# Performance work log

Measured on AMD Instinct MI355X. Metric: run time of the kernel, lower is better.

## Reference

```python
import jax, jax.numpy as jnp
import numpy as np

N_NODES = 100000
N_EDGES = 3200000
D_IN = 128


def setup_inputs() -> dict:
    key = jax.random.key(0)
    k1, k2, k3, k4 = jax.random.split(key, 4)
    x = jax.random.normal(k1, (N_NODES, D_IN), dtype=jnp.float32)
    edge_index = jax.random.randint(k2, (2, N_EDGES), 0, N_NODES, dtype=jnp.int64)
    W1 = jax.random.normal(k3, (D_IN, 16), dtype=jnp.float32) * (1.0 / np.sqrt(D_IN))
    b1 = jnp.zeros((16,), dtype=jnp.float32)
    W2 = jax.random.normal(k4, (16, 2), dtype=jnp.float32) * (1.0 / np.sqrt(16))
    b2 = jnp.zeros((2,), dtype=jnp.float32)
    return {"x": x, "edge_index": edge_index, "W1": W1, "b1": b1, "W2": W2, "b2": b2}


def _gcn_norm(edge_index, n_nodes):
    # Add self-loops, then symmetric degree normalization (PyG gcn_norm).
    loops = jnp.arange(n_nodes, dtype=edge_index.dtype)
    row = jnp.concatenate([edge_index[0], loops])  # source
    col = jnp.concatenate([edge_index[1], loops])  # target
    ones = jnp.ones(row.shape[0], dtype=jnp.float32)
    deg = jax.ops.segment_sum(ones, col, num_segments=n_nodes)
    dis = jnp.where(deg > 0, jax.lax.rsqrt(deg), 0.0)  # deg^{-1/2}
    norm = dis[row] * dis[col]  # [E+N]
    return row, col, norm


def _gcn_conv(x, row, col, norm, W, b, n_nodes):
    h = x @ W  # transform first (PyG order): [N, out]
    msgs = h[row] * norm[:, None]  # gather from source, scale
    agg = jax.ops.segment_sum(msgs, col, num_segments=n_nodes)  # scatter-add to target
    return agg + b


def reference(x, edge_index, W1, b1, W2, b2):
    n = x.shape[0]
    row, col, norm = _gcn_norm(edge_index, n)
    h = _gcn_conv(x, row, col, norm, W1, b1, n)
    h = jax.nn.relu(h)
    h = _gcn_conv(h, row, col, norm, W2, b2, n)
    return jax.nn.log_softmax(h, axis=1)
```

## Files before the change

kernel.cpp:

```cpp
#include <hip/hip_runtime.h>
#include <hip/hip_fp16.h>

#define DIN 128
#define BSH 7
#define BSIZE 128
#define NBMAX 800
#define CAP 4480
#define CHUNK 6656
#define EPT 13
#define PB 512
#define PZ 0xAAAAAAAAu

struct PlaceSmem {
    int pk[CHUNK];
    unsigned short bkid[CHUNK];
    int lcnt[NBMAX], lstart[NBMAX], gofs[NBMAX], lcur[NBMAX];
    int sst[16];
};
struct HSmem {
    float xs[64 * 132];
    float wt[16 * 132];
};
union MegaSmem {
    PlaceSmem p;
    HSmem h;
};

__global__ __launch_bounds__(PB, 6) void mega_kernel(const int* __restrict__ row,
                                                     const int* __restrict__ col,
                                                     const float* __restrict__ x,
                                                     const float* __restrict__ W1,
                                                     unsigned* __restrict__ cur,
                                                     int* __restrict__ sp,
                                                     __half* __restrict__ hp,
                                                     int E, int N, int NB, int PBLKS) {
    __shared__ MegaSmem sm;
    int t = threadIdx.x;
    int bid = blockIdx.x;

    if (bid < PBLKS) {
        int e0 = bid * CHUNK;
        int cnt = min(CHUNK, E - e0);
        bool full = (cnt == CHUNK);
        for (int i = t; i < NBMAX; i += PB) { sm.p.lcnt[i] = 0; sm.p.lcur[i] = 0; }
        __syncthreads();
        int cv[EPT], rv[EPT];
        if (full) {
            #pragma unroll
            for (int k = 0; k < EPT; k++) cv[k] = col[e0 + t + k * PB];
            #pragma unroll
            for (int k = 0; k < EPT; k++) rv[k] = row[e0 + t + k * PB];
            #pragma unroll
            for (int k = 0; k < EPT; k++) atomicAdd(&sm.p.lcnt[cv[k] >> BSH], 1);
        } else {
            for (int i = t; i < cnt; i += PB)
                atomicAdd(&sm.p.lcnt[col[e0 + i] >> BSH], 1);
        }
        __syncthreads();
        int b2i = t * 2;
        int v0 = (b2i + 0 < NBMAX) ? sm.p.lcnt[b2i + 0] : 0;
        int v1 = (b2i + 1 < NBMAX) ? sm.p.lcnt[b2i + 1] : 0;
        unsigned g0 = 0, g1 = 0;
        if (b2i + 0 < NB && v0) g0 = atomicAdd(&cur[b2i + 0], (unsigned)v0) - PZ;
        if (b2i + 1 < NB && v1) g1 = atomicAdd(&cur[b2i + 1], (unsigned)v1) - PZ;
        int tot = v0 + v1;
        int lane = t & 63, w = t >> 6;
        int sc = tot;
        #pragma unroll
        for (int d = 1; d < 64; d <<= 1) {
            int up = __shfl_up(sc, d);
            if (lane >= d) sc += up;
        }
        if (lane == 63) sm.p.sst[w] = sc;
        __syncthreads();
        if (t < 64) {
            int v = (lane < 8) ? sm.p.sst[lane] : 0;
            #pragma unroll
            for (int d = 1; d < 8; d <<= 1) {
                int up = __shfl_up(v, d);
                if (lane >= d) v += up;
            }
            if (lane < 8) sm.p.sst[8 + lane] = v;
        }
        __syncthreads();
        int wpre = (w > 0) ? sm.p.sst[8 + w - 1] : 0;
        int ex = sc + wpre - tot;
        if (b2i + 0 < NBMAX) sm.p.lstart[b2i + 0] = ex;
        if (b2i + 1 < NBMAX) sm.p.lstart[b2i + 1] = ex + v0;
        if (b2i + 0 < NB) sm.p.gofs[b2i + 0] = (b2i + 0) * CAP + (int)g0 - ex;
        if (b2i + 1 < NB) sm.p.gofs[b2i + 1] = (b2i + 1) * CAP + (int)g1 - (ex + v0);
        __syncthreads();
        if (full) {
            #pragma unroll
            for (int k = 0; k < EPT; k++) {
                int cc = cv[k];
                int b  = cc >> BSH;
                int rk = atomicAdd(&sm.p.lcur[b], 1);
                int pos = sm.p.lstart[b] + rk;
                sm.p.pk[pos]   = ((cc & (BSIZE - 1)) << 17) | rv[k];
                sm.p.bkid[pos] = (unsigned short)b;
            }
            __syncthreads();
            #pragma unroll
            for (int k = 0; k < EPT; k++) {
                int i = t + k * PB;
                sp[sm.p.gofs[sm.p.bkid[i]] + i] = sm.p.pk[i];
            }
        } else {
            for (int i = t; i < cnt; i += PB) {
                int r  = row[e0 + i];
                int cc = col[e0 + i];
                int b  = cc >> BSH;
                int rk = atomicAdd(&sm.p.lcur[b], 1);
                int pos = sm.p.lstart[b] + rk;
                sm.p.pk[pos]   = ((cc & (BSIZE - 1)) << 17) | r;
                sm.p.bkid[pos] = (unsigned short)b;
            }
            __syncthreads();
            for (int i = t; i < cnt; i += PB)
                sp[sm.p.gofs[sm.p.bkid[i]] + i] = sm.p.pk[i];
        }
    } else {
        int base = (bid - PBLKS) * 64;
        float* xs = sm.h.xs;
        float* wt = sm.h.wt;
        for (int i = t; i < DIN * 16; i += PB) {
            int d = i >> 4, k = i & 15;
            wt[k * 132 + d] = W1[i];
        }
        int nrow = min(64, N - base);
        if (nrow <= 0) return;
        for (int i = t; i < 64 * 32; i += PB) {
            int r = i >> 5, c4 = i & 31;
            float4 v = make_float4(0.f, 0.f, 0.f, 0.f);
            if (r < nrow) v = *(const float4*)(x + (size_t)(base + r) * DIN + c4 * 4);
            *(float4*)(xs + r * 132 + c4 * 4) = v;
        }
        __syncthreads();
        int r  = t >> 3;
        int k0 = (t & 7) * 2;
        const float4* xa = (const float4*)(xs + r * 132);
        const float4* wa = (const float4*)(wt + k0 * 132);
        const float4* wb = (const float4*)(wt + (k0 + 1) * 132);
        float a0 = 0.f, a1 = 0.f;
        #pragma unroll 8
        for (int d4 = 0; d4 < 32; d4++) {
            float4 va = xa[d4], u0 = wa[d4], u1 = wb[d4];
            a0 += va.x*u0.x + va.y*u0.y + va.z*u0.z + va.w*u0.w;
            a1 += va.x*u1.x + va.y*u1.y + va.z*u1.z + va.w*u1.w;
        }
        int n = base + r;
        if (n < N) {
            hp[(size_t)n * 16 + k0 + 0] = __float2half(a0);
            hp[(size_t)n * 16 + k0 + 1] = __float2half(a1);
        }
    }
}

__global__ __launch_bounds__(256) void dscale_kernel(const int* __restrict__ sp,
                                                     const unsigned* __restrict__ cur,
                                                     __half* __restrict__ hp, int N) {
    __shared__ int lcnt[BSIZE];
    __shared__ float disl[BSIZE];
    int b = blockIdx.x;
    int t = threadIdx.x;
    int cntb = (int)(cur[b] - PZ);
    const int* src = sp + (size_t)b * CAP;
    if (t < BSIZE) lcnt[t] = 0;
    __syncthreads();
    int n4 = cntb >> 2;
    const int4* src4 = (const int4*)src;
    #pragma unroll 2
    for (int i = t; i < n4; i += 256) {
        int4 v = src4[i];
        atomicAdd(&lcnt[v.x >> 17], 1);
        atomicAdd(&lcnt[v.y >> 17], 1);
        atomicAdd(&lcnt[v.z >> 17], 1);
        atomicAdd(&lcnt[v.w >> 17], 1);
    }
    for (int i = (n4 << 2) + t; i < cntb; i += 256)
        atomicAdd(&lcnt[src[i] >> 17], 1);
    __syncthreads();
    if (t < BSIZE) disl[t] = rsqrtf((float)lcnt[t] + 1.0f);
    __syncthreads();
    int r = t >> 1, part = t & 1;
    int gt = b * BSIZE + r;
    if (gt < N) {
        uint4* p = (uint4*)(hp + (size_t)gt * 16) + part;
        uint4 v = *p;
        __half2* h2 = (__half2*)&v;
        float dv = disl[r];
        #pragma unroll
        for (int q = 0; q < 4; q++) {
            float2 f = __half22float2(h2[q]);
            f.x *= dv; f.y *= dv;
            h2[q] = __float22half2_rn(f);
        }
        *p = v;
    }
}

__global__ __launch_bounds__(512) void bsg1_kernel(const int* __restrict__ sp,
                                                   const unsigned* __restrict__ cur,
                                                   const __half2* __restrict__ hp2,
                                                   const float* __restrict__ b1,
                                                   const float* __restrict__ W2,
                                                   int* __restrict__ srt2,
                                                   int* __restrict__ off,
                                                   float* __restrict__ gp, int N) {
    __shared__ int ss[CAP];
    __shared__ int lcnt[BSIZE], lstart[BSIZE], lcur[BSIZE];
    __shared__ int stot[2];
    int B = blockIdx.x;
    int t = threadIdx.x;
    int cntb = (int)(cur[B] - PZ);
    const int* reg = sp + (size_t)B * CAP;
    if (t < BSIZE) { lcnt[t] = 0; lcur[t] = 0; }
    __syncthreads();
    int rc[9];
    #pragma unroll
    for (int k = 0; k < 9; k++) {
        int i = k * 512 + t;
        rc[k] = (i < cntb) ? reg[i] : -1;
    }
    #pragma unroll
    for (int k = 0; k < 9; k++)
        if (rc[k] >= 0) atomicAdd(&lcnt[rc[k] >> 17], 1);
    __syncthreads();
    int lane = t & 63, w = t >> 6;
    int v = (t < BSIZE) ? lcnt[t] : 0;
    int sc = v;
    #pragma unroll
    for (int d = 1; d < 64; d <<= 1) {
        int up = __shfl_up(sc, d);
        if (lane >= d) sc += up;
    }
    if (t < BSIZE && lane == 63) stot[w] = sc;
    __syncthreads();
    if (t < BSIZE) lstart[t] = sc - v + ((w == 1) ? stot[0] : 0);
    __syncthreads();
    #pragma unroll
    for (int k = 0; k < 9; k++) {
        int vv = rc[k];
        if (vv >= 0) {
            int lc = vv >> 17;
            int rk = atomicAdd(&lcur[lc], 1);
            ss[lstart[lc] + rk] = vv & 0x1FFFF;
        }
    }
    __syncthreads();
    for (int i = t; i < cntb; i += 512) srt2[(size_t)B * CAP + i] = ss[i];
    if (t < BSIZE) {
        off[B * (BSIZE + 1) + t] = B * CAP + lstart[t];
    } else if (t == BSIZE) {
        off[B * (BSIZE + 1) + BSIZE] = B * CAP + cntb;
    }
    int k2  = t & 7;
    int ltg = t >> 3;
    #pragma unroll
    for (int r2 = 0; r2 < 2; r2++) {
        int lt = r2 * 64 + ltg;
        int gt = B * BSIZE + lt;
        if (gt < N) {
            int j0 = lstart[lt];
            int j1 = j0 + lcnt[lt];
            float2 acc0 = __half22float2(hp2[(size_t)gt * 8 + k2]);
            float2 acc1 = make_float2(0.f, 0.f);
            float2 acc2 = make_float2(0.f, 0.f);
            float2 acc3 = make_float2(0.f, 0.f);
            int j = j0;
            for (; j + 3 < j1; j += 4) {
                int r0 = ss[j + 0], r1 = ss[j + 1], r2i = ss[j + 2], r3 = ss[j + 3];
                float2 h0 = __half22float2(hp2[(size_t)r0 * 8 + k2]);
                float2 h1 = __half22float2(hp2[(size_t)r1 * 8 + k2]);
                float2 h2 = __half22float2(hp2[(size_t)r2i * 8 + k2]);
                float2 h3 = __half22float2(hp2[(size_t)r3 * 8 + k2]);
                acc0.x += h0.x; acc0.y += h0.y;
                acc1.x += h1.x; acc1.y += h1.y;
                acc2.x += h2.x; acc2.y += h2.y;
                acc3.x += h3.x; acc3.y += h3.y;
            }
            for (; j < j1; j++) {
                int r = ss[j];
                float2 hv = __half22float2(hp2[(size_t)r * 8 + k2]);
                acc0.x += hv.x; acc0.y += hv.y;
            }
            float2 acc = make_float2(acc0.x + acc1.x + acc2.x + acc3.x,
                                     acc0.y + acc1.y + acc2.y + acc3.y);
            float d = rsqrtf((float)lcnt[lt] + 1.0f);
            int k0 = k2 * 2;
            float v0 = fmaxf(fmaf(acc.x, d, b1[k0 + 0]), 0.0f);
            float v1 = fmaxf(fmaf(acc.y, d, b1[k0 + 1]), 0.0f);
            float p0 = v0 * W2[k0 * 2 + 0] + v1 * W2[k0 * 2 + 2];
            float p1 = v0 * W2[k0 * 2 + 1] + v1 * W2[k0 * 2 + 3];
            p0 += __shfl_xor(p0, 1); p1 += __shfl_xor(p1, 1);
            p0 += __shfl_xor(p0, 2); p1 += __shfl_xor(p1, 2);
            p0 += __shfl_xor(p0, 4); p1 += __shfl_xor(p1, 4);
            if (k2 == 0) *(float2*)(gp + (size_t)gt * 2) = make_float2(p0 * d, p1 * d);
        }
    }
}

__global__ __launch_bounds__(256) void g2_kernel(const int* __restrict__ srt2,
                                                 const int* __restrict__ off,
                                                 const float* __restrict__ gp,
                                                 const float* __restrict__ b2,
                                                 float* __restrict__ out, int N) {
    int t = blockIdx.x * 256 + threadIdx.x;
    int c    = t >> 3;
    int slot = t & 7;
    if (c >= N) return;
    int idx = (c >> 7) * (BSIZE + 1) + (c & 127);
    int j0 = off[idx];
    int j1 = off[idx + 1];
    float a0 = 0.0f, a1v = 0.0f;
    for (int j = j0 + slot; j < j1; j += 8) {
        int r = srt2[j];
        float2 gv = *(const float2*)(gp + (size_t)r * 2);
        a0  += gv.x;
        a1v += gv.y;
    }
    a0 += __shfl_xor(a0, 1); a1v += __shfl_xor(a1v, 1);
    a0 += __shfl_xor(a0, 2); a1v += __shfl_xor(a1v, 2);
    a0 += __shfl_xor(a0, 4); a1v += __shfl_xor(a1v, 4);
    if (slot == 0) {
        float2 self = *(const float2*)(gp + (size_t)c * 2);
        float d = rsqrtf((float)(j1 - j0) + 1.0f);
        float o0 = (a0  + self.x) * d + b2[0];
        float o1 = (a1v + self.y) * d + b2[1];
        float m = fmaxf(o0, o1);
        float lse = m + logf(expf(o0 - m) + expf(o1 - m));
        *(float2*)(out + (size_t)c * 2) = make_float2(o0 - lse, o1 - lse);
    }
}

extern "C" void kernel_launch(void* const* d_in, const int* in_sizes, int n_in,
                              void* d_out, int out_size, void* d_ws, size_t ws_size,
                              hipStream_t stream) {
    const float* x  = (const float*)d_in[0];
    const int*   ei = (const int*)d_in[1];
    const float* W1 = (const float*)d_in[2];
    const float* b1 = (const float*)d_in[3];
    const float* W2 = (const float*)d_in[4];
    const float* b2 = (const float*)d_in[5];
    float* out = (float*)d_out;

    const int N = in_sizes[0] / DIN;
    const int E = in_sizes[1] / 2;
    const int* row = ei;
    const int* col = ei + E;
    const int NB    = (N + BSIZE - 1) / BSIZE;
    const int PBLKS = (E + CHUNK - 1) / CHUNK;
    const int HBLKS = (N + 63) / 64;

    unsigned* cur  = (unsigned*)d_ws;
    int*      off  = (int*)(cur + NBMAX);
    int*      sp   = off + (size_t)NBMAX * (BSIZE + 1);
    int*      srt2 = sp + (size_t)NBMAX * CAP;
    __half*   hp   = (__half*)(srt2 + (size_t)NBMAX * CAP);
    float*    gp   = (float*)(hp + (size_t)N * 16);

    mega_kernel  <<<PBLKS + HBLKS, PB, 0, stream>>>(row, col, x, W1, cur, sp, hp, E, N, NB, PBLKS);
    dscale_kernel<<<NB, 256, 0, stream>>>(sp, cur, hp, N);
    bsg1_kernel  <<<NB, 512, 0, stream>>>(sp, cur, (const __half2*)hp, b1, W2, srt2, off, gp, N);
    g2_kernel    <<<(int)(((size_t)N * 8 + 255) / 256), 256, 0, stream>>>(srt2, off, gp, b2, out, N);
}
```

Before: 186.1 us.

## Restructure X@W1 GEMM so each thread computes one full row, chunked over K

The dense transform branch of the mega kernel now gives each block 512 rows and each thread one whole 16-wide output row. The thread accumulates over K in 8 chunks of 16 staged through shared memory, with W1 kept untransposed and read as broadcast float4. Output is written as two 16-byte half vectors instead of scalar half stores. This cuts the number of H blocks and redundant W1 loads and improves register reuse, at the cost of more syncs per block and less latency hiding per block.

```diff
diff --git a/kernel.cpp b/kernel.cpp
--- a/kernel.cpp
+++ b/kernel.cpp
@@ -9,6 +9,7 @@
 #define CHUNK 6656
 #define EPT 13
 #define PB 512
+#define HROWS 512
 #define PZ 0xAAAAAAAAu
 
 struct PlaceSmem {
@@ -18,8 +19,8 @@
     int sst[16];
 };
 struct HSmem {
-    float xs[64 * 132];
-    float wt[16 * 132];
+    float xs[HROWS * 20];
+    float wt[DIN * 16];
 };
 union MegaSmem {
     PlaceSmem p;
@@ -121,38 +122,65 @@
                 sp[sm.p.gofs[sm.p.bkid[i]] + i] = sm.p.pk[i];
         }
     } else {
-        int base = (bid - PBLKS) * 64;
+        int base = (bid - PBLKS) * HROWS;
         float* xs = sm.h.xs;
         float* wt = sm.h.wt;
-        for (int i = t; i < DIN * 16; i += PB) {
-            int d = i >> 4, k = i & 15;
-            wt[k * 132 + d] = W1[i];
-        }
-        int nrow = min(64, N - base);
-        if (nrow <= 0) return;
-        for (int i = t; i < 64 * 32; i += PB) {
-            int r = i >> 5, c4 = i & 31;
-            float4 v = make_float4(0.f, 0.f, 0.f, 0.f);
-            if (r < nrow) v = *(const float4*)(x + (size_t)(base + r) * DIN + c4 * 4);
-            *(float4*)(xs + r * 132 + c4 * 4) = v;
-        }
-        __syncthreads();
-        int r  = t >> 3;
-        int k0 = (t & 7) * 2;
-        const float4* xa = (const float4*)(xs + r * 132);
-        const float4* wa = (const float4*)(wt + k0 * 132);
-        const float4* wb = (const float4*)(wt + (k0 + 1) * 132);
-        float a0 = 0.f, a1 = 0.f;
-        #pragma unroll 8
-        for (int d4 = 0; d4 < 32; d4++) {
-            float4 va = xa[d4], u0 = wa[d4], u1 = wb[d4];
-            a0 += va.x*u0.x + va.y*u0.y + va.z*u0.z + va.w*u0.w;
-            a1 += va.x*u1.x + va.y*u1.y + va.z*u1.z + va.w*u1.w;
-        }
-        int n = base + r;
+        ((float4*)wt)[t] = ((const float4*)W1)[t];
+        float4 acc0 = make_float4(0.f, 0.f, 0.f, 0.f);
+        float4 acc1 = acc0, acc2 = acc0, acc3 = acc0;
+        int n = base + t;
+        for (int kc = 0; kc < 8; kc++) {
+            if (kc) __syncthreads();
+            #pragma unroll
+            for (int q = 0; q < 4; q++) {
+                int f = q * 512 + t;
+                int r = f >> 2, c = f & 3;
+                int g = base + r;
+                float4 v = make_float4(0.f, 0.f, 0.f, 0.f);
+                if (g < N) v = *(const float4*)(x + (size_t)g * DIN + kc * 16 + c * 4);
+                *(float4*)(xs + r * 20 + c * 4) = v;
+            }
+            __syncthreads();
+            float4 xv0 = *(const float4*)(xs + t * 20 + 0);
+            float4 xv1 = *(const float4*)(xs + t * 20 + 4);
+            float4 xv2 = *(const float4*)(xs + t * 20 + 8);
+            float4 xv3 = *(const float4*)(xs + t * 20 + 12);
+            const float4* Wc = (const float4*)wt + kc * 64;
+            #pragma unroll
+            for (int q = 0; q < 4; q++) {
+                float4 xq = (q == 0) ? xv0 : (q == 1) ? xv1 : (q == 2) ? xv2 : xv3;
+                #pragma unroll
+                for (int kk = 0; kk < 4; kk++) {
+                    float xk = (kk == 0) ? xq.x : (kk == 1) ? xq.y : (kk == 2) ? xq.z : xq.w;
+                    int krow = q * 4 + kk;
+                    float4 w0 = Wc[krow * 4 + 0];
+                    float4 w1 = Wc[krow * 4 + 1];
+                    float4 w2 = Wc[krow * 4 + 2];
+                    float4 w3 = Wc[krow * 4 + 3];
+                    acc0.x = fmaf(xk, w0.x, acc0.x); acc0.y = fmaf(xk, w0.y, acc0.y);
+                    acc0.z = fmaf(xk, w0.z, acc0.z); acc0.w = fmaf(xk, w0.w, acc0.w);
+                    acc1.x = fmaf(xk, w1.x, acc1.x); acc1.y = fmaf(xk, w1.y, acc1.y);
+                    acc1.z = fmaf(xk, w1.z, acc1.z); acc1.w = fmaf(xk, w1.w, acc1.w);
+                    acc2.x = fmaf(xk, w2.x, acc2.x); acc2.y = fmaf(xk, w2.y, acc2.y);
+                    acc2.z = fmaf(xk, w2.z, acc2.z); acc2.w = fmaf(xk, w2.w, acc2.w);
+                    acc3.x = fmaf(xk, w3.x, acc3.x); acc3.y = fmaf(xk, w3.y, acc3.y);
+                    acc3.z = fmaf(xk, w3.z, acc3.z); acc3.w = fmaf(xk, w3.w, acc3.w);
+                }
+            }
+        }
         if (n < N) {
-            hp[(size_t)n * 16 + k0 + 0] = __float2half(a0);
-            hp[(size_t)n * 16 + k0 + 1] = __float2half(a1);
+            union { __half2 h2[8]; uint4 u4[2]; } ob;
+            ob.h2[0] = __floats2half2_rn(acc0.x, acc0.y);
+            ob.h2[1] = __floats2half2_rn(acc0.z, acc0.w);
+            ob.h2[2] = __floats2half2_rn(acc1.x, acc1.y);
+            ob.h2[3] = __floats2half2_rn(acc1.z, acc1.w);
+            ob.h2[4] = __floats2half2_rn(acc2.x, acc2.y);
+            ob.h2[5] = __floats2half2_rn(acc2.z, acc2.w);
+            ob.h2[6] = __floats2half2_rn(acc3.x, acc3.y);
+            ob.h2[7] = __floats2half2_rn(acc3.z, acc3.w);
+            uint4* o = (uint4*)(hp + (size_t)n * 16);
+            o[0] = ob.u4[0];
+            o[1] = ob.u4[1];
         }
     }
 }
@@ -351,7 +379,7 @@
     const int* col = ei + E;
     const int NB    = (N + BSIZE - 1) / BSIZE;
     const int PBLKS = (E + CHUNK - 1) / CHUNK;
-    const int HBLKS = (N + 63) / 64;
+    const int HBLKS = (N + HROWS - 1) / HROWS;
 
     unsigned* cur  = (unsigned*)d_ws;
     int*      off  = (int*)(cur + NBMAX);
```

New measurement: 203.0 us. 1.09x slower.
